# Optimization experiments

Hardware: AMD Instinct MI355X
Metric: run time of the kernel (lower is better)

The kernel has to match this reference:

```python
import jax, jax.numpy as jnp
import numpy as np
from jax import lax

D_MODEL, D_INNER, D_STATE, D_CONV, DT_RANK = 1024, 2048, 16, 4, 64
B_SZ, L = 2, 2048


def silu(v):
    return v * jax.nn.sigmoid(v)


def setup_inputs() -> dict:
    key = jax.random.key(0)
    ks = jax.random.split(key, 9)
    s = 0.02
    x = jax.random.normal(ks[0], (B_SZ, L, D_MODEL), jnp.float32)
    W_in = jax.random.normal(ks[1], (D_MODEL, 2 * D_INNER), jnp.float32) * s
    conv_w = jax.random.normal(ks[2], (D_INNER, D_CONV), jnp.float32) * 0.1  # depthwise kernel
    conv_b = jax.random.normal(ks[3], (D_INNER,), jnp.float32) * 0.01
    W_xproj = jax.random.normal(ks[4], (D_INNER, DT_RANK + 2 * D_STATE), jnp.float32) * s
    W_dt = jax.random.normal(ks[5], (DT_RANK, D_INNER), jnp.float32) * s
    b_dt = jax.random.normal(ks[6], (D_INNER,), jnp.float32) * 0.01
    A_log = jnp.log(jnp.tile(jnp.arange(1, D_STATE + 1, dtype=jnp.float32), (D_INNER, 1)))
    D = jnp.ones((D_INNER,), jnp.float32)
    W_out = jax.random.normal(ks[7], (D_INNER, D_MODEL), jnp.float32) * s
    return dict(x=x, W_in=W_in, conv_w=conv_w, conv_b=conv_b, W_xproj=W_xproj,
                W_dt=W_dt, b_dt=b_dt, A_log=A_log, D=D, W_out=W_out)


def reference(x, W_in, conv_w, conv_b, W_xproj, W_dt, b_dt, A_log, D, W_out):
    # in_proj, split into conv path u and gate res
    xr = x @ W_in                                  # (B, L, 2*d_inner)
    u, res = jnp.split(xr, 2, axis=-1)
    # causal depthwise conv1d (left-pad d_conv-1), then SiLU
    uc = jnp.swapaxes(u, 1, 2)                     # (B, C, L)
    uc = lax.conv_general_dilated(
        uc, conv_w[:, None, :], window_strides=(1,),
        padding=[(D_CONV - 1, 0)], feature_group_count=D_INNER,
        dimension_numbers=('NCH', 'OIH', 'NCH'))
    uc = uc + conv_b[None, :, None]
    u = silu(jnp.swapaxes(uc, 1, 2))               # (B, L, d_inner)
    # S6 projections
    x_dbl = u @ W_xproj                            # (B, L, dt_rank + 2*N)
    dt_low = x_dbl[..., :DT_RANK]
    Bm = x_dbl[..., DT_RANK:DT_RANK + D_STATE]     # (B, L, N)
    Cm = x_dbl[..., DT_RANK + D_STATE:]            # (B, L, N)
    dt = jax.nn.softplus(dt_low @ W_dt + b_dt)     # (B, L, d_inner)
    A = -jnp.exp(A_log)                            # (d_inner, N)
    # selective scan over time
    def step(h, inp):
        dt_t, B_t, C_t, u_t = inp                  # (B,d), (B,N), (B,N), (B,d)
        dA = jnp.exp(dt_t[:, :, None] * A)         # (B, d, N)
        dBu = dt_t[:, :, None] * B_t[:, None, :] * u_t[:, :, None]
        h = dA * h + dBu
        y = jnp.sum(h * C_t[:, None, :], axis=-1)  # (B, d)
        return h, y
    h0 = jnp.zeros((B_SZ, D_INNER, D_STATE), u.dtype)
    xs = (jnp.swapaxes(dt, 0, 1), jnp.swapaxes(Bm, 0, 1),
          jnp.swapaxes(Cm, 0, 1), jnp.swapaxes(u, 0, 1))
    _, ys = lax.scan(step, h0, xs)
    y = jnp.swapaxes(ys, 0, 1) + u * D             # (B, L, d_inner)
    # gate and out_proj
    y = y * silu(res)
    return y @ W_out
```

## Files before the change

kernel.cpp:

```cpp
#include <hip/hip_runtime.h>
#include <cstdint>
#include <cstddef>

#define DMODEL 1024
#define DINNER 2048
#define DSTATE 16
#define DCONV  4
#define DTRANK 64
#define BSZ    2
#define SEQL   2048
#define MROWS  (BSZ*SEQL)
#define NCHUNK 32
#define CLEN   (SEQL/NCHUNK)

typedef __bf16 bf16;
typedef bf16  bf16x8 __attribute__((ext_vector_type(8)));
typedef bf16  bf16x4 __attribute__((ext_vector_type(4)));
typedef float floatx4 __attribute__((ext_vector_type(4)));

#define EPILDC 136

__device__ __forceinline__ float fsigmoid(float x){ return 1.f/(1.f+__expf(-x)); }
__device__ __forceinline__ float fsilu(float x){ return x*fsigmoid(x); }

__device__ __forceinline__ void gload_lds16(const void* g, void* l){
  __builtin_amdgcn_global_load_lds((__attribute__((address_space(1))) void*)g,
                                   (__attribute__((address_space(3))) void*)l,
                                   16, 0, 0);
}

__global__ void k_cast_bf16(const float* __restrict__ in, bf16* __restrict__ out, int n){
  int i = (blockIdx.x*blockDim.x + threadIdx.x)*4;
  if (i < n){
    float4 v = *(const float4*)(in + i);
    bf16x4 o; o[0]=(bf16)v.x; o[1]=(bf16)v.y; o[2]=(bf16)v.z; o[3]=(bf16)v.w;
    *(bf16x4*)(out + i) = o;
  }
}

__global__ void k_transpose_all(const float* __restrict__ W_in, const float* __restrict__ W_out,
                                const float* __restrict__ W_xproj, const float* __restrict__ W_dt,
                                bf16* __restrict__ WinT, bf16* __restrict__ WoutT,
                                bf16* __restrict__ WxT, bf16* __restrict__ WdtT){
  __shared__ float tile[32][33];
  int b = blockIdx.x;
  const float* in; bf16* out; int R, C, outR, nbx;
  if      (b < 4096)            { in=W_in;    out=WinT;  R=1024; C=4096; outR=4096; nbx=128; }
  else if (b < 4096+2048)       { b-=4096;    in=W_out;  out=WoutT; R=2048; C=1024; outR=1024; nbx=32; }
  else if (b < 4096+2048+256)   { b-=6144;    in=W_xproj;out=WxT;  R=2048; C=96;   outR=128;  nbx=4; }
  else                          { b-=6400;    in=W_dt;   out=WdtT; R=64;   C=2048; outR=2048; nbx=64; }
  int c0 = (b % nbx)*32, r0 = (b / nbx)*32;
  int tx = threadIdx.x, ty = threadIdx.y;
  #pragma unroll
  for (int ii=0; ii<4; ++ii){
    int r = r0 + ty + ii*8, c = c0 + tx;
    float v = 0.f;
    if (r < R && c < C) v = in[(size_t)r*C + c];
    tile[ty+ii*8][tx] = v;
  }
  __syncthreads();
  #pragma unroll
  for (int ii=0; ii<4; ++ii){
    int orow = c0 + ty + ii*8;
    int ocol = r0 + tx;
    if (orow < outR && ocol < R) out[(size_t)orow*R + ocol] = (bf16)tile[tx][ty+ii*8];
  }
}

template<int EPI>
__global__ __launch_bounds__(256)
void k_gemm_bt(const bf16* __restrict__ A, const bf16* __restrict__ Bt,
               int M, int N, int K,
               float* __restrict__ C0, bf16* __restrict__ C1, bf16* __restrict__ C2,
               const float* __restrict__ bias){
  __shared__ bf16 lds[17408];
  const int tid  = threadIdx.x;
  const int lane = tid & 63;
  const int wave = tid >> 6;
  const int quad = lane >> 4;
  const int mrow = lane & 15;
  const int wr = wave >> 1, wc = wave & 1;
  const int bm = blockIdx.y * 128, bn = blockIdx.x * 128;
  const int Ks   = K / gridDim.z;
  const int kbeg = blockIdx.z * Ks;

  floatx4 acc[4][4];
  #pragma unroll
  for (int i=0;i<4;++i)
    #pragma unroll
    for (int j=0;j<4;++j) acc[i][j] = (floatx4){0.f,0.f,0.f,0.f};

  const int ar0 = tid >> 2;
  const int kc  = ((tid & 3) ^ ((ar0 >> 1) & 3)) * 8;
  const bf16* Ag0 = A  + (size_t)(bm + ar0)      * K + kc;
  const bf16* Ag1 = A  + (size_t)(bm + ar0 + 64) * K + kc;
  const bf16* Bg0 = Bt + (size_t)(bn + ar0)      * K + kc;
  const bf16* Bg1 = Bt + (size_t)(bn + ar0 + 64) * K + kc;
  const int ksl = (mrow >> 1) & 3;

  auto stage = [&](int k0, int p){
    bf16* bA = lds + p*4096;
    bf16* bB = lds + 8192 + p*4096;
    gload_lds16(Ag0 + k0, bA + (size_t)tid*8);
    gload_lds16(Ag1 + k0, bA + (size_t)(256+tid)*8);
    gload_lds16(Bg0 + k0, bB + (size_t)tid*8);
    gload_lds16(Bg1 + k0, bB + (size_t)(256+tid)*8);
  };

  stage(kbeg, 0);
  int p = 0;
  for (int k0 = kbeg; k0 < kbeg + Ks; k0 += 32){
    __syncthreads();
    if (k0 + 32 < kbeg + Ks) stage(k0 + 32, p ^ 1);
    const bf16* bA = lds + p*4096;
    const bf16* bB = lds + 8192 + p*4096;
    bf16x8 af[4], bfr[4];
    #pragma unroll
    for (int i=0;i<4;++i)
      af[i] = *(const bf16x8*)(bA + (wr*64 + i*16 + mrow)*32 + (quad ^ ksl)*8);
    #pragma unroll
    for (int j=0;j<4;++j)
      bfr[j] = *(const bf16x8*)(bB + (wc*64 + j*16 + mrow)*32 + (quad ^ ksl)*8);
    #pragma unroll
    for (int i=0;i<4;++i)
      #pragma unroll
      for (int j=0;j<4;++j)
        acc[i][j] = __builtin_amdgcn_mfma_f32_16x16x32_bf16(af[i], bfr[j], acc[i][j], 0,0,0);
    p ^= 1;
  }

  if (EPI == 0){
    float* Cz = C0 + (size_t)blockIdx.z * M * N;
    #pragma unroll
    for (int i=0;i<4;++i){
      #pragma unroll
      for (int r=0;r<4;++r){
        int row = bm + wr*64 + i*16 + quad*4 + r;
        #pragma unroll
        for (int j=0;j<4;++j){
          int col = bn + wc*64 + j*16 + mrow;
          Cz[(size_t)row*N + col] = acc[i][j][r];
        }
      }
    }
  } else {
    __syncthreads();
    const bool isres = (EPI == 1) && (bn >= DINNER);
    #pragma unroll
    for (int i=0;i<4;++i)
      #pragma unroll
      for (int r=0;r<4;++r){
        int lrow = wr*64 + i*16 + quad*4 + r;
        #pragma unroll
        for (int j=0;j<4;++j){
          int lcol = wc*64 + j*16 + mrow;
          float v = acc[i][j][r];
          float vt;
          if (EPI == 1) vt = isres ? fsilu(v) : v;
          else {
            float z = v + bias[bn + lcol];
            vt = (z > 20.f) ? z : log1pf(__expf(z));
          }
          lds[lrow*EPILDC + lcol] = (bf16)vt;
        }
      }
    __syncthreads();
    bf16* dst; int ldc;
    if (EPI == 1){ ldc = DINNER; dst = isres ? (C2 + (bn - DINNER)) : (C1 + bn); }
    else         { ldc = N;      dst = C1 + bn; }
    const int rr = tid >> 1, hh = (tid & 1)*64;
    #pragma unroll
    for (int i=0;i<8;++i)
      *(bf16x8*)(dst + (size_t)(bm + rr)*ldc + hh + i*8) =
        *(const bf16x8*)(lds + rr*EPILDC + hh + i*8);
  }
}

__global__ void k_xdbl_reduce(const float* __restrict__ part, float* __restrict__ xdbl,
                              bf16* __restrict__ dtlowb){
  int t = blockIdx.x*blockDim.x + threadIdx.x;
  int i4 = t*4;
  floatx4 acc = (floatx4){0.f,0.f,0.f,0.f};
  #pragma unroll
  for (int z=0; z<8; ++z)
    acc += *(const floatx4*)(part + (size_t)z*MROWS*128 + i4);
  *(floatx4*)(xdbl + i4) = acc;
  int r = i4 >> 7, c = i4 & 127;
  if (c < DTRANK){
    bf16x4 o; o[0]=(bf16)acc[0]; o[1]=(bf16)acc[1]; o[2]=(bf16)acc[2]; o[3]=(bf16)acc[3];
    *(bf16x4*)(dtlowb + (size_t)r*DTRANK + c) = o;
  }
}

__global__ void k_out_reduce(const float* __restrict__ part, float* __restrict__ out){
  int i4 = (blockIdx.x*blockDim.x + threadIdx.x)*4;
  floatx4 a = *(const floatx4*)(part + i4);
  floatx4 b = *(const floatx4*)(part + (size_t)MROWS*DMODEL + i4);
  *(floatx4*)(out + i4) = a + b;
}

__global__ void k_conv_silu(const bf16* __restrict__ u_pre,
                            const float* __restrict__ conv_w,
                            const float* __restrict__ conv_b,
                            bf16* __restrict__ ub){
  int t   = blockIdx.x*blockDim.x + threadIdx.x;
  int d4  = (t & (DINNER/4-1))*4;
  int row = t >> 9;
  int l   = row & (SEQL-1);
  float4 cb = *(const float4*)(conv_b + d4);
  float acc[4] = {cb.x, cb.y, cb.z, cb.w};
  float4 w0 = *(const float4*)(conv_w + (d4+0)*4);
  float4 w1 = *(const float4*)(conv_w + (d4+1)*4);
  float4 w2 = *(const float4*)(conv_w + (d4+2)*4);
  float4 w3 = *(const float4*)(conv_w + (d4+3)*4);
  float wk[4][4] = {{w0.x,w0.y,w0.z,w0.w},{w1.x,w1.y,w1.z,w1.w},
                    {w2.x,w2.y,w2.z,w2.w},{w3.x,w3.y,w3.z,w3.w}};
  #pragma unroll
  for (int k=0;k<4;++k){
    int lk = l + k - 3;
    if (lk >= 0){
      bf16x4 uv = *(const bf16x4*)(u_pre + (size_t)(row + k - 3)*DINNER + d4);
      #pragma unroll
      for (int j=0;j<4;++j) acc[j] += (float)uv[j] * wk[j][k];
    }
  }
  bf16x4 o;
  #pragma unroll
  for (int j=0;j<4;++j) o[j] = (bf16)fsilu(acc[j]);
  *(bf16x4*)(ub + (size_t)row*DINNER + d4) = o;
}

__global__ void k_scan_phase1(const bf16* __restrict__ dt, const bf16* __restrict__ ub,
                              const float* __restrict__ x_dbl, const float* __restrict__ A_log,
                              float* __restrict__ Pbuf, float* __restrict__ Sbuf){
  int t  = blockIdx.x*blockDim.x + threadIdx.x;
  int g  = t & 3;
  int d  = (t >> 2) & (DINNER-1);
  int bc = t >> 13;
  int c  = bc & (NCHUNK-1);
  int b  = bc >> 5;
  floatx4 alog = *(const floatx4*)(A_log + d*DSTATE + g*4);
  float an[4];
  #pragma unroll
  for (int n=0;n<4;++n) an[n] = -__expf(alog[n]);
  float P[4] = {1.f,1.f,1.f,1.f}, S[4] = {0.f,0.f,0.f,0.f};
  int base_row = b*SEQL + c*CLEN;
  for (int s=0;s<CLEN;++s){
    size_t row = base_row + s;
    float dtv = (float)dt[row*DINNER + d];
    float uv  = (float)ub[row*DINNER + d];
    float du  = dtv*uv;
    floatx4 Bv = *(const floatx4*)(x_dbl + row*128 + DTRANK + g*4);
    #pragma unroll
    for (int n=0;n<4;++n){
      float e = __expf(dtv*an[n]);
      P[n] *= e;
      S[n]  = fmaf(S[n], e, du*Bv[n]);
    }
  }
  size_t ob = ((size_t)bc*DINNER + d)*DSTATE + g*4;
  floatx4 Pv = {P[0],P[1],P[2],P[3]}, Sv = {S[0],S[1],S[2],S[3]};
  *(floatx4*)(Pbuf + ob) = Pv;
  *(floatx4*)(Sbuf + ob) = Sv;
}

__global__ void k_scan_phase2(const float* __restrict__ Pbuf, float* __restrict__ Sbuf){
  int t = blockIdx.x*blockDim.x + threadIdx.x;
  int b   = t >> 15;
  int rem = t & 32767;
  float h = 0.f;
  for (int c=0;c<NCHUNK;++c){
    size_t ix = (size_t)(b*NCHUNK + c)*DINNER*DSTATE + rem;
    float p = Pbuf[ix], s = Sbuf[ix];
    Sbuf[ix] = h;
    h = fmaf(p, h, s);
  }
}

__global__ void k_scan_phase3(const bf16* __restrict__ dt, const bf16* __restrict__ ub,
                              const float* __restrict__ x_dbl, const float* __restrict__ A_log,
                              const float* __restrict__ Dvec, const float* __restrict__ Hin,
                              const bf16* __restrict__ resb, bf16* __restrict__ yb){
  int t  = blockIdx.x*blockDim.x + threadIdx.x;
  int g  = t & 3;
  int d  = (t >> 2) & (DINNER-1);
  int bc = t >> 13;
  int c  = bc & (NCHUNK-1);
  int b  = bc >> 5;
  floatx4 alog = *(const floatx4*)(A_log + d*DSTATE + g*4);
  float an[4];
  #pragma unroll
  for (int n=0;n<4;++n) an[n] = -__expf(alog[n]);
  floatx4 h = *(const floatx4*)(Hin + ((size_t)bc*DINNER + d)*DSTATE + g*4);
  float Dd = Dvec[d];
  int base_row = b*SEQL + c*CLEN;
  for (int s=0;s<CLEN;++s){
    size_t row = base_row + s;
    float dtv = (float)dt[row*DINNER + d];
    float uv  = (float)ub[row*DINNER + d];
    float du  = dtv*uv;
    floatx4 Bv = *(const floatx4*)(x_dbl + row*128 + DTRANK + g*4);
    floatx4 Cv = *(const floatx4*)(x_dbl + row*128 + DTRANK + DSTATE + g*4);
    float y = 0.f;
    #pragma unroll
    for (int n=0;n<4;++n){
      float e = __expf(dtv*an[n]);
      h[n] = fmaf(h[n], e, du*Bv[n]);
      y = fmaf(h[n], Cv[n], y);
    }
    y += __shfl_xor(y, 1);
    y += __shfl_xor(y, 2);
    if (g == 0){
      y = (y + uv*Dd) * (float)resb[row*DINNER + d];
      yb[row*DINNER + d] = (bf16)y;
    }
  }
}

extern "C" void kernel_launch(void* const* d_in, const int* in_sizes, int n_in,
                              void* d_out, int out_size, void* d_ws, size_t ws_size,
                              hipStream_t stream){
  const float* x      = (const float*)d_in[0];
  const float* W_in   = (const float*)d_in[1];
  const float* conv_w = (const float*)d_in[2];
  const float* conv_b = (const float*)d_in[3];
  const float* W_xproj= (const float*)d_in[4];
  const float* W_dt   = (const float*)d_in[5];
  const float* b_dt   = (const float*)d_in[6];
  const float* A_log  = (const float*)d_in[7];
  const float* Dv     = (const float*)d_in[8];
  const float* W_out  = (const float*)d_in[9];
  float* out = (float*)d_out;

  uint8_t* wp = (uint8_t*)d_ws;
  auto alloc = [&](size_t bytes)->void*{ void* p = wp; wp += (bytes + 255) & ~(size_t)255; return p; };
  bf16*  xb     = (bf16*) alloc((size_t)MROWS*DMODEL*2);
  bf16*  WinT   = (bf16*) alloc((size_t)2*DINNER*DMODEL*2);
  bf16*  WoutT  = (bf16*) alloc((size_t)DMODEL*DINNER*2);
  bf16*  WxT    = (bf16*) alloc((size_t)128*DINNER*2);
  bf16*  WdtT   = (bf16*) alloc((size_t)DINNER*DTRANK*2);
  bf16*  updt   = (bf16*) alloc((size_t)MROWS*DINNER*2);
  float* scanPS = (float*)alloc((size_t)2*BSZ*NCHUNK*DSTATE*DINNER*4);
  float* Pbuf   = scanPS;
  float* Sbuf   = scanPS + (size_t)BSZ*NCHUNK*DSTATE*DINNER;
  float* xdbl_part = scanPS;
  float* outpart   = (float*)updt;
  bf16*  resb   = (bf16*) alloc((size_t)MROWS*DINNER*2);
  bf16*  ub     = (bf16*) alloc((size_t)MROWS*DINNER*2);
  float* xdbl   = (float*)alloc((size_t)MROWS*128*4);
  bf16*  dtlowb = (bf16*) alloc((size_t)MROWS*DTRANK*2);
  bf16*  yb     = (bf16*) alloc((size_t)MROWS*DINNER*2);

  k_cast_bf16<<<(MROWS*DMODEL/4 + 255)/256, 256, 0, stream>>>(x, xb, MROWS*DMODEL);
  k_transpose_all<<<4096+2048+256+128, dim3(32,8), 0, stream>>>(W_in, W_out, W_xproj, W_dt,
                                                                WinT, WoutT, WxT, WdtT);

  k_gemm_bt<1><<<dim3(4096/128, 4096/128), 256, 0, stream>>>(xb, WinT, MROWS, 2*DINNER, DMODEL, nullptr, updt, resb, nullptr);
  k_conv_silu<<<MROWS*DINNER/4/256, 256, 0, stream>>>(updt, conv_w, conv_b, ub);
  k_gemm_bt<0><<<dim3(1, 4096/128, 8), 256, 0, stream>>>(ub, WxT, MROWS, 128, DINNER, xdbl_part, nullptr, nullptr, nullptr);
  k_xdbl_reduce<<<(MROWS*128/4)/256, 256, 0, stream>>>(xdbl_part, xdbl, dtlowb);
  k_gemm_bt<2><<<dim3(2048/128, 4096/128), 256, 0, stream>>>(dtlowb, WdtT, MROWS, DINNER, DTRANK, nullptr, updt, nullptr, b_dt);
  k_scan_phase1<<<BSZ*NCHUNK*DINNER*4/256, 256, 0, stream>>>(updt, ub, xdbl, A_log, Pbuf, Sbuf);
  k_scan_phase2<<<BSZ*DINNER*DSTATE/256, 256, 0, stream>>>(Pbuf, Sbuf);
  k_scan_phase3<<<BSZ*NCHUNK*DINNER*4/256, 256, 0, stream>>>(updt, ub, xdbl, A_log, Dv, Sbuf, resb, yb);
  k_gemm_bt<0><<<dim3(1024/128, 4096/128, 2), 256, 0, stream>>>(yb, WoutT, MROWS, DMODEL, DINNER, outpart, nullptr, nullptr, nullptr);
  k_out_reduce<<<(MROWS*DMODEL/4)/256, 256, 0, stream>>>(outpart, out);
}
```

Before: 364.3 us.

## Use 256x128-tile GEMM for in/out projections, fuse prep kernels, split-K 4

Adds a new bf16 MFMA GEMM with 256x128 block tiles, 128x64 per wave and launch bounds of two blocks per CU. It replaces the older 128x128 kernel for the input and output projections, aiming for more data reuse per LDS load. The x cast and the weight transposes are merged into one prep kernel to drop a launch. The output projection now uses split-K 4 with a 4-way reduce, and workspace buffers are reordered so the larger partial-sum buffer aliases updt, scanPS, resb and ub, all dead by then. The risks are register pressure from 128 accumulators per lane and the extra partial-sum traffic.

Measured after the change: 372.9 us. 1.02x slower.

```diff
diff --git a/kernel.cpp b/kernel.cpp
--- a/kernel.cpp
+++ b/kernel.cpp
@@ -29,28 +29,28 @@
                                    16, 0, 0);
 }
 
-__global__ void k_cast_bf16(const float* __restrict__ in, bf16* __restrict__ out, int n){
-  int i = (blockIdx.x*blockDim.x + threadIdx.x)*4;
-  if (i < n){
-    float4 v = *(const float4*)(in + i);
-    bf16x4 o; o[0]=(bf16)v.x; o[1]=(bf16)v.y; o[2]=(bf16)v.z; o[3]=(bf16)v.w;
-    *(bf16x4*)(out + i) = o;
-  }
-}
-
-__global__ void k_transpose_all(const float* __restrict__ W_in, const float* __restrict__ W_out,
-                                const float* __restrict__ W_xproj, const float* __restrict__ W_dt,
-                                bf16* __restrict__ WinT, bf16* __restrict__ WoutT,
-                                bf16* __restrict__ WxT, bf16* __restrict__ WdtT){
+__global__ void k_prep(const float* __restrict__ x, bf16* __restrict__ xb,
+                       const float* __restrict__ W_in, const float* __restrict__ W_out,
+                       const float* __restrict__ W_xproj, const float* __restrict__ W_dt,
+                       bf16* __restrict__ WinT, bf16* __restrict__ WoutT,
+                       bf16* __restrict__ WxT, bf16* __restrict__ WdtT){
   __shared__ float tile[32][33];
   int b = blockIdx.x;
+  if (b < 4096){
+    int i = (b*256 + threadIdx.x)*4;
+    float4 v = *(const float4*)(x + i);
+    bf16x4 o; o[0]=(bf16)v.x; o[1]=(bf16)v.y; o[2]=(bf16)v.z; o[3]=(bf16)v.w;
+    *(bf16x4*)(xb + i) = o;
+    return;
+  }
+  b -= 4096;
   const float* in; bf16* out; int R, C, outR, nbx;
   if      (b < 4096)            { in=W_in;    out=WinT;  R=1024; C=4096; outR=4096; nbx=128; }
   else if (b < 4096+2048)       { b-=4096;    in=W_out;  out=WoutT; R=2048; C=1024; outR=1024; nbx=32; }
   else if (b < 4096+2048+256)   { b-=6144;    in=W_xproj;out=WxT;  R=2048; C=96;   outR=128;  nbx=4; }
   else                          { b-=6400;    in=W_dt;   out=WdtT; R=64;   C=2048; outR=2048; nbx=64; }
   int c0 = (b % nbx)*32, r0 = (b / nbx)*32;
-  int tx = threadIdx.x, ty = threadIdx.y;
+  int tx = threadIdx.x & 31, ty = threadIdx.x >> 5;
   #pragma unroll
   for (int ii=0; ii<4; ++ii){
     int r = r0 + ty + ii*8, c = c0 + tx;
@@ -64,6 +64,111 @@
     int orow = c0 + ty + ii*8;
     int ocol = r0 + tx;
     if (orow < outR && ocol < R) out[(size_t)orow*R + ocol] = (bf16)tile[tx][ty+ii*8];
+  }
+}
+
+template<int EPI>
+__global__ __launch_bounds__(256, 2)
+void k_gemm2(const bf16* __restrict__ A, const bf16* __restrict__ Bt,
+             int M, int N, int K,
+             float* __restrict__ C0, bf16* __restrict__ C1, bf16* __restrict__ C2){
+  __shared__ bf16 lds[24576];
+  const int tid  = threadIdx.x;
+  const int lane = tid & 63;
+  const int wave = tid >> 6;
+  const int quad = lane >> 4;
+  const int mrow = lane & 15;
+  const int wrow = (wave >> 1) * 128, wcol = (wave & 1) * 64;
+  const int bm = blockIdx.y * 256, bn = blockIdx.x * 128;
+  const int Ks   = K / gridDim.z;
+  const int kbeg = blockIdx.z * Ks;
+
+  floatx4 acc[8][4];
+  #pragma unroll
+  for (int i=0;i<8;++i)
+    #pragma unroll
+    for (int j=0;j<4;++j) acc[i][j] = (floatx4){0.f,0.f,0.f,0.f};
+
+  const int r_loc = tid >> 2;
+  const int kc    = ((tid & 3) ^ ((r_loc >> 1) & 3)) * 8;
+  const bf16* Ag = A  + (size_t)(bm + r_loc) * K + kc;
+  const bf16* Bg = Bt + (size_t)(bn + r_loc) * K + kc;
+  const int ksl = (mrow >> 1) & 3;
+
+  auto stage = [&](int k0, int p){
+    bf16* bA = lds + p*12288;
+    bf16* bB = bA + 8192;
+    #pragma unroll
+    for (int s=0;s<4;++s)
+      gload_lds16(Ag + k0 + (size_t)s*64*K, bA + (s*256 + tid)*8);
+    #pragma unroll
+    for (int s=0;s<2;++s)
+      gload_lds16(Bg + k0 + (size_t)s*64*K, bB + (s*256 + tid)*8);
+  };
+
+  stage(kbeg, 0);
+  int p = 0;
+  for (int k0 = kbeg; k0 < kbeg + Ks; k0 += 32){
+    __syncthreads();
+    if (k0 + 32 < kbeg + Ks) stage(k0 + 32, p ^ 1);
+    const bf16* bA = lds + p*12288;
+    const bf16* bB = bA + 8192;
+    bf16x8 af[8], bfr[4];
+    #pragma unroll
+    for (int i=0;i<8;++i)
+      af[i] = *(const bf16x8*)(bA + (wrow + i*16 + mrow)*32 + (quad ^ ksl)*8);
+    #pragma unroll
+    for (int j=0;j<4;++j)
+      bfr[j] = *(const bf16x8*)(bB + (wcol + j*16 + mrow)*32 + (quad ^ ksl)*8);
+    #pragma unroll
+    for (int i=0;i<8;++i)
+      #pragma unroll
+      for (int j=0;j<4;++j)
+        acc[i][j] = __builtin_amdgcn_mfma_f32_16x16x32_bf16(af[i], bfr[j], acc[i][j], 0,0,0);
+    p ^= 1;
+  }
+
+  if (EPI == 0){
+    float* Cz = C0 + (size_t)blockIdx.z * M * N;
+    #pragma unroll
+    for (int i=0;i<8;++i)
+      #pragma unroll
+      for (int r=0;r<4;++r){
+        int row = bm + wrow + i*16 + quad*4 + r;
+        #pragma unroll
+        for (int j=0;j<4;++j){
+          int col = bn + wcol + j*16 + mrow;
+          Cz[(size_t)row*N + col] = acc[i][j][r];
+        }
+      }
+  } else {
+    const bool isres = (bn >= DINNER);
+    bf16* dst = isres ? (C2 + (bn - DINNER)) : (C1 + bn);
+    __syncthreads();
+    #pragma unroll
+    for (int hp=0; hp<2; ++hp){
+      if (hp) __syncthreads();
+      if ((wave >> 1) == hp){
+        #pragma unroll
+        for (int i=0;i<8;++i)
+          #pragma unroll
+          for (int r=0;r<4;++r){
+            int lrow = i*16 + quad*4 + r;
+            #pragma unroll
+            for (int j=0;j<4;++j){
+              int lcol = wcol + j*16 + mrow;
+              float v = acc[i][j][r];
+              lds[lrow*EPILDC + lcol] = (bf16)(isres ? fsilu(v) : v);
+            }
+          }
+      }
+      __syncthreads();
+      const int rr = tid >> 1, hh = (tid & 1)*64;
+      #pragma unroll
+      for (int i=0;i<8;++i)
+        *(bf16x8*)(dst + (size_t)(bm + hp*128 + rr)*DINNER + hh + i*8) =
+          *(const bf16x8*)(lds + rr*EPILDC + hh + i*8);
+    }
   }
 }
 
@@ -192,11 +297,13 @@
   }
 }
 
-__global__ void k_out_reduce(const float* __restrict__ part, float* __restrict__ out){
+__global__ void k_out_reduce4(const float* __restrict__ part, float* __restrict__ out){
   int i4 = (blockIdx.x*blockDim.x + threadIdx.x)*4;
   floatx4 a = *(const floatx4*)(part + i4);
-  floatx4 b = *(const floatx4*)(part + (size_t)MROWS*DMODEL + i4);
-  *(floatx4*)(out + i4) = a + b;
+  #pragma unroll
+  for (int z=1; z<4; ++z)
+    a += *(const floatx4*)(part + (size_t)z*MROWS*DMODEL + i4);
+  *(floatx4*)(out + i4) = a;
 }
 
 __global__ void k_conv_silu(const bf16* __restrict__ u_pre,
@@ -341,21 +448,20 @@
   bf16*  WdtT   = (bf16*) alloc((size_t)DINNER*DTRANK*2);
   bf16*  updt   = (bf16*) alloc((size_t)MROWS*DINNER*2);
   float* scanPS = (float*)alloc((size_t)2*BSZ*NCHUNK*DSTATE*DINNER*4);
+  bf16*  resb   = (bf16*) alloc((size_t)MROWS*DINNER*2);
+  bf16*  ub     = (bf16*) alloc((size_t)MROWS*DINNER*2);
   float* Pbuf   = scanPS;
   float* Sbuf   = scanPS + (size_t)BSZ*NCHUNK*DSTATE*DINNER;
   float* xdbl_part = scanPS;
   float* outpart   = (float*)updt;
-  bf16*  resb   = (bf16*) alloc((size_t)MROWS*DINNER*2);
-  bf16*  ub     = (bf16*) alloc((size_t)MROWS*DINNER*2);
   float* xdbl   = (float*)alloc((size_t)MROWS*128*4);
   bf16*  dtlowb = (bf16*) alloc((size_t)MROWS*DTRANK*2);
   bf16*  yb     = (bf16*) alloc((size_t)MROWS*DINNER*2);
 
-  k_cast_bf16<<<(MROWS*DMODEL/4 + 255)/256, 256, 0, stream>>>(x, xb, MROWS*DMODEL);
-  k_transpose_all<<<4096+2048+256+128, dim3(32,8), 0, stream>>>(W_in, W_out, W_xproj, W_dt,
-                                                                WinT, WoutT, WxT, WdtT);
-
-  k_gemm_bt<1><<<dim3(4096/128, 4096/128), 256, 0, stream>>>(xb, WinT, MROWS, 2*DINNER, DMODEL, nullptr, updt, resb, nullptr);
+  k_prep<<<4096 + 4096+2048+256+128, 256, 0, stream>>>(x, xb, W_in, W_out, W_xproj, W_dt,
+                                                       WinT, WoutT, WxT, WdtT);
+
+  k_gemm2<1><<<dim3(4096/128, 4096/256), 256, 0, stream>>>(xb, WinT, MROWS, 2*DINNER, DMODEL, nullptr, updt, resb);
   k_conv_silu<<<MROWS*DINNER/4/256, 256, 0, stream>>>(updt, conv_w, conv_b, ub);
   k_gemm_bt<0><<<dim3(1, 4096/128, 8), 256, 0, stream>>>(ub, WxT, MROWS, 128, DINNER, xdbl_part, nullptr, nullptr, nullptr);
   k_xdbl_reduce<<<(MROWS*128/4)/256, 256, 0, stream>>>(xdbl_part, xdbl, dtlowb);
@@ -363,6 +469,6 @@
   k_scan_phase1<<<BSZ*NCHUNK*DINNER*4/256, 256, 0, stream>>>(updt, ub, xdbl, A_log, Pbuf, Sbuf);
   k_scan_phase2<<<BSZ*DINNER*DSTATE/256, 256, 0, stream>>>(Pbuf, Sbuf);
   k_scan_phase3<<<BSZ*NCHUNK*DINNER*4/256, 256, 0, stream>>>(updt, ub, xdbl, A_log, Dv, Sbuf, resb, yb);
-  k_gemm_bt<0><<<dim3(1024/128, 4096/128, 2), 256, 0, stream>>>(yb, WoutT, MROWS, DMODEL, DINNER, outpart, nullptr, nullptr, nullptr);
-  k_out_reduce<<<(MROWS*DMODEL/4)/256, 256, 0, stream>>>(outpart, out);
-}
+  k_gemm2<0><<<dim3(1024/128, 4096/256, 4), 256, 0, stream>>>(yb, WoutT, MROWS, DMODEL, DINNER, outpart, nullptr, nullptr);
+  k_out_reduce4<<<(MROWS*DMODEL/4)/256, 256, 0, stream>>>(outpart, out);
+}
```

## Store scan inputs channel-major via swapped GEMM operands for vectorized time loads

Applied to the files above, without the earlier changes.

The in_proj and dt GEMMs now swap their A/B operands, so they produce u, res and dt transposed (channel-major, time contiguous). The conv kernel reads the transposed u, writes both transposed and row-major outputs through a swizzled LDS tile, and the scan phases load 8 timesteps per vector load instead of one strided bf16 per step. The cast and weight-transpose kernels are merged into one prep launch. This targets the uncoalesced per-step loads in the scan, at the cost of an extra transposed copy of u and a changed GEMM epilogue.

New measurement: 461.9 us. 1.27x slower.

```diff
diff --git a/kernel.cpp b/kernel.cpp
--- a/kernel.cpp
+++ b/kernel.cpp
@@ -29,28 +29,28 @@
                                    16, 0, 0);
 }
 
-__global__ void k_cast_bf16(const float* __restrict__ in, bf16* __restrict__ out, int n){
-  int i = (blockIdx.x*blockDim.x + threadIdx.x)*4;
-  if (i < n){
-    float4 v = *(const float4*)(in + i);
-    bf16x4 o; o[0]=(bf16)v.x; o[1]=(bf16)v.y; o[2]=(bf16)v.z; o[3]=(bf16)v.w;
-    *(bf16x4*)(out + i) = o;
-  }
-}
-
-__global__ void k_transpose_all(const float* __restrict__ W_in, const float* __restrict__ W_out,
-                                const float* __restrict__ W_xproj, const float* __restrict__ W_dt,
-                                bf16* __restrict__ WinT, bf16* __restrict__ WoutT,
-                                bf16* __restrict__ WxT, bf16* __restrict__ WdtT){
+__global__ void k_prep(const float* __restrict__ x, bf16* __restrict__ xb,
+                       const float* __restrict__ W_in, const float* __restrict__ W_out,
+                       const float* __restrict__ W_xproj, const float* __restrict__ W_dt,
+                       bf16* __restrict__ WinT, bf16* __restrict__ WoutT,
+                       bf16* __restrict__ WxT, bf16* __restrict__ WdtT){
   __shared__ float tile[32][33];
   int b = blockIdx.x;
+  if (b < 4096){
+    int i = (b*256 + threadIdx.x)*4;
+    float4 v = *(const float4*)(x + i);
+    bf16x4 o; o[0]=(bf16)v.x; o[1]=(bf16)v.y; o[2]=(bf16)v.z; o[3]=(bf16)v.w;
+    *(bf16x4*)(xb + i) = o;
+    return;
+  }
+  b -= 4096;
   const float* in; bf16* out; int R, C, outR, nbx;
   if      (b < 4096)            { in=W_in;    out=WinT;  R=1024; C=4096; outR=4096; nbx=128; }
   else if (b < 4096+2048)       { b-=4096;    in=W_out;  out=WoutT; R=2048; C=1024; outR=1024; nbx=32; }
   else if (b < 4096+2048+256)   { b-=6144;    in=W_xproj;out=WxT;  R=2048; C=96;   outR=128;  nbx=4; }
   else                          { b-=6400;    in=W_dt;   out=WdtT; R=64;   C=2048; outR=2048; nbx=64; }
   int c0 = (b % nbx)*32, r0 = (b / nbx)*32;
-  int tx = threadIdx.x, ty = threadIdx.y;
+  int tx = threadIdx.x & 31, ty = threadIdx.x >> 5;
   #pragma unroll
   for (int ii=0; ii<4; ++ii){
     int r = r0 + ty + ii*8, c = c0 + tx;
@@ -145,7 +145,7 @@
     }
   } else {
     __syncthreads();
-    const bool isres = (EPI == 1) && (bn >= DINNER);
+    const bool isres = (EPI == 1) && (bm >= DINNER);
     #pragma unroll
     for (int i=0;i<4;++i)
       #pragma unroll
@@ -158,20 +158,21 @@
           float vt;
           if (EPI == 1) vt = isres ? fsilu(v) : v;
           else {
-            float z = v + bias[bn + lcol];
+            float z = v + bias[bm + lrow];
             vt = (z > 20.f) ? z : log1pf(__expf(z));
           }
           lds[lrow*EPILDC + lcol] = (bf16)vt;
         }
       }
     __syncthreads();
-    bf16* dst; int ldc;
-    if (EPI == 1){ ldc = DINNER; dst = isres ? (C2 + (bn - DINNER)) : (C1 + bn); }
-    else         { ldc = N;      dst = C1 + bn; }
+    bf16* dst;
+    if (EPI == 1) dst = isres ? (C2 + (size_t)(bm - DINNER)*MROWS) : (C1 + (size_t)bm*MROWS);
+    else          dst = C1 + (size_t)bm*MROWS;
+    dst += bn;
     const int rr = tid >> 1, hh = (tid & 1)*64;
     #pragma unroll
     for (int i=0;i<8;++i)
-      *(bf16x8*)(dst + (size_t)(bm + rr)*ldc + hh + i*8) =
+      *(bf16x8*)(dst + (size_t)rr*MROWS + hh + i*8) =
         *(const bf16x8*)(lds + rr*EPILDC + hh + i*8);
   }
 }
@@ -199,38 +200,54 @@
   *(floatx4*)(out + i4) = a + b;
 }
 
-__global__ void k_conv_silu(const bf16* __restrict__ u_pre,
-                            const float* __restrict__ conv_w,
-                            const float* __restrict__ conv_b,
-                            bf16* __restrict__ ub){
-  int t   = blockIdx.x*blockDim.x + threadIdx.x;
-  int d4  = (t & (DINNER/4-1))*4;
-  int row = t >> 9;
-  int l   = row & (SEQL-1);
-  float4 cb = *(const float4*)(conv_b + d4);
-  float acc[4] = {cb.x, cb.y, cb.z, cb.w};
-  float4 w0 = *(const float4*)(conv_w + (d4+0)*4);
-  float4 w1 = *(const float4*)(conv_w + (d4+1)*4);
-  float4 w2 = *(const float4*)(conv_w + (d4+2)*4);
-  float4 w3 = *(const float4*)(conv_w + (d4+3)*4);
-  float wk[4][4] = {{w0.x,w0.y,w0.z,w0.w},{w1.x,w1.y,w1.z,w1.w},
-                    {w2.x,w2.y,w2.z,w2.w},{w3.x,w3.y,w3.z,w3.w}};
-  #pragma unroll
-  for (int k=0;k<4;++k){
-    int lk = l + k - 3;
-    if (lk >= 0){
-      bf16x4 uv = *(const bf16x4*)(u_pre + (size_t)(row + k - 3)*DINNER + d4);
-      #pragma unroll
-      for (int j=0;j<4;++j) acc[j] += (float)uv[j] * wk[j][k];
-    }
-  }
-  bf16x4 o;
-  #pragma unroll
-  for (int j=0;j<4;++j) o[j] = (bf16)fsilu(acc[j]);
-  *(bf16x4*)(ub + (size_t)row*DINNER + d4) = o;
-}
-
-__global__ void k_scan_phase1(const bf16* __restrict__ dt, const bf16* __restrict__ ub,
+__global__ void k_conv2(const bf16* __restrict__ upreT,
+                        const float* __restrict__ conv_w, const float* __restrict__ conv_b,
+                        bf16* __restrict__ ubT, bf16* __restrict__ ub){
+  __shared__ bf16 tile[64*64];
+  const int r0 = blockIdx.x * 64;
+  const int d0 = blockIdx.y * 64;
+  const int t  = threadIdx.x;
+  const int dloc = t & 63, q = t >> 6;
+  const int d = d0 + dloc;
+  const int s = r0 + q*16;
+  const bf16* src = upreT + (size_t)d*MROWS + s;
+  bf16x8 a0 = *(const bf16x8*)(src - 8);
+  bf16x8 a1 = *(const bf16x8*)(src);
+  bf16x8 a2 = *(const bf16x8*)(src + 8);
+  float v[24];
+  #pragma unroll
+  for (int j=0;j<8;++j){ v[j]=(float)a0[j]; v[8+j]=(float)a1[j]; v[16+j]=(float)a2[j]; }
+  if ((s & (SEQL-1)) == 0){ v[5]=0.f; v[6]=0.f; v[7]=0.f; }
+  float4 w = *(const float4*)(conv_w + d*4);
+  float cb = conv_b[d];
+  float o[16];
+  #pragma unroll
+  for (int i=0;i<16;++i)
+    o[i] = fsilu(cb + w.x*v[i+5] + w.y*v[i+6] + w.z*v[i+7] + w.w*v[i+8]);
+  bf16x8 o0, o1;
+  #pragma unroll
+  for (int j=0;j<8;++j){ o0[j]=(bf16)o[j]; o1[j]=(bf16)o[8+j]; }
+  *(bf16x8*)(ubT + (size_t)d*MROWS + s)     = o0;
+  *(bf16x8*)(ubT + (size_t)d*MROWS + s + 8) = o1;
+  #pragma unroll
+  for (int i=0;i<16;++i){
+    int c = q*16 + i;
+    tile[dloc*64 + (c ^ dloc)] = (bf16)o[i];
+  }
+  __syncthreads();
+  const int rloc = t >> 2, seg = t & 3;
+  bf16x8 p0, p1;
+  #pragma unroll
+  for (int i=0;i<8;++i){
+    int dp0 = seg*16 + i, dp1 = seg*16 + 8 + i;
+    p0[i] = tile[dp0*64 + (rloc ^ dp0)];
+    p1[i] = tile[dp1*64 + (rloc ^ dp1)];
+  }
+  *(bf16x8*)(ub + (size_t)(r0 + rloc)*DINNER + d0 + seg*16)     = p0;
+  *(bf16x8*)(ub + (size_t)(r0 + rloc)*DINNER + d0 + seg*16 + 8) = p1;
+}
+
+__global__ void k_scan_phase1(const bf16* __restrict__ dtT, const bf16* __restrict__ ubT,
                               const float* __restrict__ x_dbl, const float* __restrict__ A_log,
                               float* __restrict__ Pbuf, float* __restrict__ Sbuf){
   int t  = blockIdx.x*blockDim.x + threadIdx.x;
@@ -245,17 +262,23 @@
   for (int n=0;n<4;++n) an[n] = -__expf(alog[n]);
   float P[4] = {1.f,1.f,1.f,1.f}, S[4] = {0.f,0.f,0.f,0.f};
   int base_row = b*SEQL + c*CLEN;
-  for (int s=0;s<CLEN;++s){
-    size_t row = base_row + s;
-    float dtv = (float)dt[row*DINNER + d];
-    float uv  = (float)ub[row*DINNER + d];
-    float du  = dtv*uv;
-    floatx4 Bv = *(const floatx4*)(x_dbl + row*128 + DTRANK + g*4);
-    #pragma unroll
-    for (int n=0;n<4;++n){
-      float e = __expf(dtv*an[n]);
-      P[n] *= e;
-      S[n]  = fmaf(S[n], e, du*Bv[n]);
+  const bf16* dtp = dtT + (size_t)d*MROWS + base_row;
+  const bf16* ubp = ubT + (size_t)d*MROWS + base_row;
+  for (int s8=0; s8<CLEN; s8+=8){
+    bf16x8 dt8 = *(const bf16x8*)(dtp + s8);
+    bf16x8 ub8 = *(const bf16x8*)(ubp + s8);
+    #pragma unroll
+    for (int i=0;i<8;++i){
+      size_t row = base_row + s8 + i;
+      float dtv = (float)dt8[i];
+      float du  = dtv * (float)ub8[i];
+      floatx4 Bv = *(const floatx4*)(x_dbl + row*128 + DTRANK + g*4);
+      #pragma unroll
+      for (int n=0;n<4;++n){
+        float e = __expf(dtv*an[n]);
+        P[n] *= e;
+        S[n]  = fmaf(S[n], e, du*Bv[n]);
+      }
     }
   }
   size_t ob = ((size_t)bc*DINNER + d)*DSTATE + g*4;
@@ -277,10 +300,10 @@
   }
 }
 
-__global__ void k_scan_phase3(const bf16* __restrict__ dt, const bf16* __restrict__ ub,
+__global__ void k_scan_phase3(const bf16* __restrict__ dtT, const bf16* __restrict__ ubT,
                               const float* __restrict__ x_dbl, const float* __restrict__ A_log,
                               const float* __restrict__ Dvec, const float* __restrict__ Hin,
-                              const bf16* __restrict__ resb, bf16* __restrict__ yb){
+                              const bf16* __restrict__ resbT, bf16* __restrict__ yb){
   int t  = blockIdx.x*blockDim.x + threadIdx.x;
   int g  = t & 3;
   int d  = (t >> 2) & (DINNER-1);
@@ -294,25 +317,34 @@
   floatx4 h = *(const floatx4*)(Hin + ((size_t)bc*DINNER + d)*DSTATE + g*4);
   float Dd = Dvec[d];
   int base_row = b*SEQL + c*CLEN;
-  for (int s=0;s<CLEN;++s){
-    size_t row = base_row + s;
-    float dtv = (float)dt[row*DINNER + d];
-    float uv  = (float)ub[row*DINNER + d];
-    float du  = dtv*uv;
-    floatx4 Bv = *(const floatx4*)(x_dbl + row*128 + DTRANK + g*4);
-    floatx4 Cv = *(const floatx4*)(x_dbl + row*128 + DTRANK + DSTATE + g*4);
-    float y = 0.f;
-    #pragma unroll
-    for (int n=0;n<4;++n){
-      float e = __expf(dtv*an[n]);
-      h[n] = fmaf(h[n], e, du*Bv[n]);
-      y = fmaf(h[n], Cv[n], y);
-    }
-    y += __shfl_xor(y, 1);
-    y += __shfl_xor(y, 2);
-    if (g == 0){
-      y = (y + uv*Dd) * (float)resb[row*DINNER + d];
-      yb[row*DINNER + d] = (bf16)y;
+  const bf16* dtp = dtT   + (size_t)d*MROWS + base_row;
+  const bf16* ubp = ubT   + (size_t)d*MROWS + base_row;
+  const bf16* rsp = resbT + (size_t)d*MROWS + base_row;
+  for (int s8=0; s8<CLEN; s8+=8){
+    bf16x8 dt8 = *(const bf16x8*)(dtp + s8);
+    bf16x8 ub8 = *(const bf16x8*)(ubp + s8);
+    bf16x8 rs8 = *(const bf16x8*)(rsp + s8);
+    #pragma unroll
+    for (int i=0;i<8;++i){
+      size_t row = base_row + s8 + i;
+      float dtv = (float)dt8[i];
+      float uv  = (float)ub8[i];
+      float du  = dtv*uv;
+      floatx4 Bv = *(const floatx4*)(x_dbl + row*128 + DTRANK + g*4);
+      floatx4 Cv = *(const floatx4*)(x_dbl + row*128 + DTRANK + DSTATE + g*4);
+      float y = 0.f;
+      #pragma unroll
+      for (int n=0;n<4;++n){
+        float e = __expf(dtv*an[n]);
+        h[n] = fmaf(h[n], e, du*Bv[n]);
+        y = fmaf(h[n], Cv[n], y);
+      }
+      y += __shfl_xor(y, 1);
+      y += __shfl_xor(y, 2);
+      if (g == 0){
+        y = (y + uv*Dd) * (float)rs8[i];
+        yb[row*DINNER + d] = (bf16)y;
+      }
     }
   }
 }
@@ -339,30 +371,30 @@
   bf16*  WoutT  = (bf16*) alloc((size_t)DMODEL*DINNER*2);
   bf16*  WxT    = (bf16*) alloc((size_t)128*DINNER*2);
   bf16*  WdtT   = (bf16*) alloc((size_t)DINNER*DTRANK*2);
-  bf16*  updt   = (bf16*) alloc((size_t)MROWS*DINNER*2);
+  bf16*  updtT  = (bf16*) alloc((size_t)MROWS*DINNER*2);
   float* scanPS = (float*)alloc((size_t)2*BSZ*NCHUNK*DSTATE*DINNER*4);
   float* Pbuf   = scanPS;
   float* Sbuf   = scanPS + (size_t)BSZ*NCHUNK*DSTATE*DINNER;
   float* xdbl_part = scanPS;
-  float* outpart   = (float*)updt;
-  bf16*  resb   = (bf16*) alloc((size_t)MROWS*DINNER*2);
+  float* outpart   = (float*)updtT;
+  bf16*  resbT  = (bf16*) alloc((size_t)MROWS*DINNER*2);
+  bf16*  ubT    = (bf16*) alloc((size_t)MROWS*DINNER*2);
   bf16*  ub     = (bf16*) alloc((size_t)MROWS*DINNER*2);
   float* xdbl   = (float*)alloc((size_t)MROWS*128*4);
   bf16*  dtlowb = (bf16*) alloc((size_t)MROWS*DTRANK*2);
   bf16*  yb     = (bf16*) alloc((size_t)MROWS*DINNER*2);
 
-  k_cast_bf16<<<(MROWS*DMODEL/4 + 255)/256, 256, 0, stream>>>(x, xb, MROWS*DMODEL);
-  k_transpose_all<<<4096+2048+256+128, dim3(32,8), 0, stream>>>(W_in, W_out, W_xproj, W_dt,
-                                                                WinT, WoutT, WxT, WdtT);
-
-  k_gemm_bt<1><<<dim3(4096/128, 4096/128), 256, 0, stream>>>(xb, WinT, MROWS, 2*DINNER, DMODEL, nullptr, updt, resb, nullptr);
-  k_conv_silu<<<MROWS*DINNER/4/256, 256, 0, stream>>>(updt, conv_w, conv_b, ub);
+  k_prep<<<4096 + 4096+2048+256+128, 256, 0, stream>>>(x, xb, W_in, W_out, W_xproj, W_dt,
+                                                       WinT, WoutT, WxT, WdtT);
+
+  k_gemm_bt<1><<<dim3(4096/128, 4096/128), 256, 0, stream>>>(WinT, xb, 2*DINNER, MROWS, DMODEL, nullptr, updtT, resbT, nullptr);
+  k_conv2<<<dim3(MROWS/64, DINNER/64), 256, 0, stream>>>(updtT, conv_w, conv_b, ubT, ub);
   k_gemm_bt<0><<<dim3(1, 4096/128, 8), 256, 0, stream>>>(ub, WxT, MROWS, 128, DINNER, xdbl_part, nullptr, nullptr, nullptr);
   k_xdbl_reduce<<<(MROWS*128/4)/256, 256, 0, stream>>>(xdbl_part, xdbl, dtlowb);
-  k_gemm_bt<2><<<dim3(2048/128, 4096/128), 256, 0, stream>>>(dtlowb, WdtT, MROWS, DINNER, DTRANK, nullptr, updt, nullptr, b_dt);
-  k_scan_phase1<<<BSZ*NCHUNK*DINNER*4/256, 256, 0, stream>>>(updt, ub, xdbl, A_log, Pbuf, Sbuf);
+  k_gemm_bt<2><<<dim3(4096/128, 2048/128), 256, 0, stream>>>(WdtT, dtlowb, DINNER, MROWS, DTRANK, nullptr, updtT, nullptr, b_dt);
+  k_scan_phase1<<<BSZ*NCHUNK*DINNER*4/256, 256, 0, stream>>>(updtT, ubT, xdbl, A_log, Pbuf, Sbuf);
   k_scan_phase2<<<BSZ*DINNER*DSTATE/256, 256, 0, stream>>>(Pbuf, Sbuf);
-  k_scan_phase3<<<BSZ*NCHUNK*DINNER*4/256, 256, 0, stream>>>(updt, ub, xdbl, A_log, Dv, Sbuf, resb, yb);
+  k_scan_phase3<<<BSZ*NCHUNK*DINNER*4/256, 256, 0, stream>>>(updtT, ubT, xdbl, A_log, Dv, Sbuf, resbT, yb);
   k_gemm_bt<0><<<dim3(1024/128, 4096/128, 2), 256, 0, stream>>>(yb, WoutT, MROWS, DMODEL, DINNER, outpart, nullptr, nullptr, nullptr);
   k_out_reduce<<<(MROWS*DMODEL/4)/256, 256, 0, stream>>>(outpart, out);
 }
```

## Stage scan chunk inputs in LDS and merge prep kernels into one launch

Applied to the files above, without the earlier changes.

The scan phase 1 and phase 3 kernels now cooperatively load each block's 64-row by 64-channel tile of dt, u (and the gate res in phase 3) into shared memory with 16-byte vector loads. The sequential time loop then reads these values from LDS instead of doing strided 2-byte global loads on every step. The input cast and weight-transpose kernels are also merged into one launch to save a kernel launch. The cost is extra LDS per block, which may limit occupancy, plus a block-wide barrier before the loop.

Measured after the change: 363.8 us. Within noise of the previous version (-0.1%).

```diff
diff --git a/kernel.cpp b/kernel.cpp
--- a/kernel.cpp
+++ b/kernel.cpp
@@ -19,6 +19,7 @@
 typedef float floatx4 __attribute__((ext_vector_type(4)));
 
 #define EPILDC 136
+#define SLDC   72
 
 __device__ __forceinline__ float fsigmoid(float x){ return 1.f/(1.f+__expf(-x)); }
 __device__ __forceinline__ float fsilu(float x){ return x*fsigmoid(x); }
@@ -29,28 +30,28 @@
                                    16, 0, 0);
 }
 
-__global__ void k_cast_bf16(const float* __restrict__ in, bf16* __restrict__ out, int n){
-  int i = (blockIdx.x*blockDim.x + threadIdx.x)*4;
-  if (i < n){
-    float4 v = *(const float4*)(in + i);
-    bf16x4 o; o[0]=(bf16)v.x; o[1]=(bf16)v.y; o[2]=(bf16)v.z; o[3]=(bf16)v.w;
-    *(bf16x4*)(out + i) = o;
-  }
-}
-
-__global__ void k_transpose_all(const float* __restrict__ W_in, const float* __restrict__ W_out,
-                                const float* __restrict__ W_xproj, const float* __restrict__ W_dt,
-                                bf16* __restrict__ WinT, bf16* __restrict__ WoutT,
-                                bf16* __restrict__ WxT, bf16* __restrict__ WdtT){
+__global__ void k_prep(const float* __restrict__ x, bf16* __restrict__ xb,
+                       const float* __restrict__ W_in, const float* __restrict__ W_out,
+                       const float* __restrict__ W_xproj, const float* __restrict__ W_dt,
+                       bf16* __restrict__ WinT, bf16* __restrict__ WoutT,
+                       bf16* __restrict__ WxT, bf16* __restrict__ WdtT){
   __shared__ float tile[32][33];
   int b = blockIdx.x;
+  if (b < 4096){
+    int i = (b*256 + threadIdx.x)*4;
+    float4 v = *(const float4*)(x + i);
+    bf16x4 o; o[0]=(bf16)v.x; o[1]=(bf16)v.y; o[2]=(bf16)v.z; o[3]=(bf16)v.w;
+    *(bf16x4*)(xb + i) = o;
+    return;
+  }
+  b -= 4096;
   const float* in; bf16* out; int R, C, outR, nbx;
   if      (b < 4096)            { in=W_in;    out=WinT;  R=1024; C=4096; outR=4096; nbx=128; }
   else if (b < 4096+2048)       { b-=4096;    in=W_out;  out=WoutT; R=2048; C=1024; outR=1024; nbx=32; }
   else if (b < 4096+2048+256)   { b-=6144;    in=W_xproj;out=WxT;  R=2048; C=96;   outR=128;  nbx=4; }
   else                          { b-=6400;    in=W_dt;   out=WdtT; R=64;   C=2048; outR=2048; nbx=64; }
   int c0 = (b % nbx)*32, r0 = (b / nbx)*32;
-  int tx = threadIdx.x, ty = threadIdx.y;
+  int tx = threadIdx.x & 31, ty = threadIdx.x >> 5;
   #pragma unroll
   for (int ii=0; ii<4; ++ii){
     int r = r0 + ty + ii*8, c = c0 + tx;
@@ -233,23 +234,36 @@
 __global__ void k_scan_phase1(const bf16* __restrict__ dt, const bf16* __restrict__ ub,
                               const float* __restrict__ x_dbl, const float* __restrict__ A_log,
                               float* __restrict__ Pbuf, float* __restrict__ Sbuf){
-  int t  = blockIdx.x*blockDim.x + threadIdx.x;
+  __shared__ bf16 sdt[64*SLDC], sub[64*SLDC];
+  const int tid = threadIdx.x;
+  int t  = blockIdx.x*256 + tid;
   int g  = t & 3;
   int d  = (t >> 2) & (DINNER-1);
+  int dloc = d & 63, d0 = d & ~63;
   int bc = t >> 13;
   int c  = bc & (NCHUNK-1);
   int b  = bc >> 5;
+  int base_row = b*SEQL + c*CLEN;
+  {
+    int r = tid >> 2, ch = (tid & 3)*16;
+    const bf16* gd = dt + (size_t)(base_row + r)*DINNER + d0 + ch;
+    const bf16* gu = ub + (size_t)(base_row + r)*DINNER + d0 + ch;
+    *(bf16x8*)(sdt + r*SLDC + ch)     = *(const bf16x8*)(gd);
+    *(bf16x8*)(sdt + r*SLDC + ch + 8) = *(const bf16x8*)(gd + 8);
+    *(bf16x8*)(sub + r*SLDC + ch)     = *(const bf16x8*)(gu);
+    *(bf16x8*)(sub + r*SLDC + ch + 8) = *(const bf16x8*)(gu + 8);
+  }
   floatx4 alog = *(const floatx4*)(A_log + d*DSTATE + g*4);
   float an[4];
   #pragma unroll
   for (int n=0;n<4;++n) an[n] = -__expf(alog[n]);
+  __syncthreads();
   float P[4] = {1.f,1.f,1.f,1.f}, S[4] = {0.f,0.f,0.f,0.f};
-  int base_row = b*SEQL + c*CLEN;
-  for (int s=0;s<CLEN;++s){
+  #pragma unroll 8
+  for (int s=0; s<CLEN; ++s){
+    float dtv = (float)sdt[s*SLDC + dloc];
+    float du  = dtv * (float)sub[s*SLDC + dloc];
     size_t row = base_row + s;
-    float dtv = (float)dt[row*DINNER + d];
-    float uv  = (float)ub[row*DINNER + d];
-    float du  = dtv*uv;
     floatx4 Bv = *(const floatx4*)(x_dbl + row*128 + DTRANK + g*4);
     #pragma unroll
     for (int n=0;n<4;++n){
@@ -281,24 +295,41 @@
                               const float* __restrict__ x_dbl, const float* __restrict__ A_log,
                               const float* __restrict__ Dvec, const float* __restrict__ Hin,
                               const bf16* __restrict__ resb, bf16* __restrict__ yb){
-  int t  = blockIdx.x*blockDim.x + threadIdx.x;
+  __shared__ bf16 sdt[64*SLDC], sub[64*SLDC], srs[64*SLDC];
+  const int tid = threadIdx.x;
+  int t  = blockIdx.x*256 + tid;
   int g  = t & 3;
   int d  = (t >> 2) & (DINNER-1);
+  int dloc = d & 63, d0 = d & ~63;
   int bc = t >> 13;
   int c  = bc & (NCHUNK-1);
   int b  = bc >> 5;
+  int base_row = b*SEQL + c*CLEN;
+  {
+    int r = tid >> 2, ch = (tid & 3)*16;
+    const bf16* gd = dt   + (size_t)(base_row + r)*DINNER + d0 + ch;
+    const bf16* gu = ub   + (size_t)(base_row + r)*DINNER + d0 + ch;
+    const bf16* gr = resb + (size_t)(base_row + r)*DINNER + d0 + ch;
+    *(bf16x8*)(sdt + r*SLDC + ch)     = *(const bf16x8*)(gd);
+    *(bf16x8*)(sdt + r*SLDC + ch + 8) = *(const bf16x8*)(gd + 8);
+    *(bf16x8*)(sub + r*SLDC + ch)     = *(const bf16x8*)(gu);
+    *(bf16x8*)(sub + r*SLDC + ch + 8) = *(const bf16x8*)(gu + 8);
+    *(bf16x8*)(srs + r*SLDC + ch)     = *(const bf16x8*)(gr);
+    *(bf16x8*)(srs + r*SLDC + ch + 8) = *(const bf16x8*)(gr + 8);
+  }
   floatx4 alog = *(const floatx4*)(A_log + d*DSTATE + g*4);
   float an[4];
   #pragma unroll
   for (int n=0;n<4;++n) an[n] = -__expf(alog[n]);
   floatx4 h = *(const floatx4*)(Hin + ((size_t)bc*DINNER + d)*DSTATE + g*4);
   float Dd = Dvec[d];
-  int base_row = b*SEQL + c*CLEN;
-  for (int s=0;s<CLEN;++s){
+  __syncthreads();
+  #pragma unroll 8
+  for (int s=0; s<CLEN; ++s){
+    float dtv = (float)sdt[s*SLDC + dloc];
+    float uv  = (float)sub[s*SLDC + dloc];
+    float du  = dtv*uv;
     size_t row = base_row + s;
-    float dtv = (float)dt[row*DINNER + d];
-    float uv  = (float)ub[row*DINNER + d];
-    float du  = dtv*uv;
     floatx4 Bv = *(const floatx4*)(x_dbl + row*128 + DTRANK + g*4);
     floatx4 Cv = *(const floatx4*)(x_dbl + row*128 + DTRANK + DSTATE + g*4);
     float y = 0.f;
@@ -311,7 +342,7 @@
     y += __shfl_xor(y, 1);
     y += __shfl_xor(y, 2);
     if (g == 0){
-      y = (y + uv*Dd) * (float)resb[row*DINNER + d];
+      y = (y + uv*Dd) * (float)srs[s*SLDC + dloc];
       yb[row*DINNER + d] = (bf16)y;
     }
   }
@@ -351,9 +382,8 @@
   bf16*  dtlowb = (bf16*) alloc((size_t)MROWS*DTRANK*2);
   bf16*  yb     = (bf16*) alloc((size_t)MROWS*DINNER*2);
 
-  k_cast_bf16<<<(MROWS*DMODEL/4 + 255)/256, 256, 0, stream>>>(x, xb, MROWS*DMODEL);
-  k_transpose_all<<<4096+2048+256+128, dim3(32,8), 0, stream>>>(W_in, W_out, W_xproj, W_dt,
-                                                                WinT, WoutT, WxT, WdtT);
+  k_prep<<<4096 + 4096+2048+256+128, 256, 0, stream>>>(x, xb, W_in, W_out, W_xproj, W_dt,
+                                                       WinT, WoutT, WxT, WdtT);
 
   k_gemm_bt<1><<<dim3(4096/128, 4096/128), 256, 0, stream>>>(xb, WinT, MROWS, 2*DINNER, DMODEL, nullptr, updt, resb, nullptr);
   k_conv_silu<<<MROWS*DINNER/4/256, 256, 0, stream>>>(updt, conv_w, conv_b, ub);
```
